# Performance work log

Measured on AMD Instinct MI355X. Metric: run time of the kernel, lower is better.

## Reference

```python
import jax, jax.numpy as jnp
import numpy as np
import math

B, S, D, H = 2, 2048, 1024, 16
DH = D // H  # head_size = 64


def setup_inputs() -> dict:
    key = jax.random.key(0)
    ks = jax.random.split(key, 11)
    s = 0.02
    return {
        "queries": jax.random.normal(ks[0], (B, S, D), jnp.float32),
        "keys": jax.random.normal(ks[1], (B, S, D), jnp.float32),
        "values": jax.random.normal(ks[2], (B, S, D), jnp.float32),
        # nn.Linear weights: y = x @ W.T + b, W has shape (out, in)
        "W_Q": jax.random.normal(ks[3], (D, D), jnp.float32) * s,
        "b_Q": jax.random.normal(ks[4], (D,), jnp.float32) * s,
        "W_K": jax.random.normal(ks[5], (D, D), jnp.float32) * s,
        "b_K": jax.random.normal(ks[6], (D,), jnp.float32) * s,
        "W_V": jax.random.normal(ks[7], (D, D), jnp.float32) * s,
        "b_V": jax.random.normal(ks[8], (D,), jnp.float32) * s,
        "W_O": jax.random.normal(ks[9], (D, D), jnp.float32) * s,
        "b_O": jax.random.normal(ks[10], (D,), jnp.float32) * s,
    }


def _split_heads(x):
    # (B, S, H*DH) -> (B, H, S, DH); torch.chunk+stack == reshape+transpose
    b, s, _ = x.shape
    return x.reshape(b, s, H, DH).transpose(0, 2, 1, 3)


def reference(queries, keys, values, W_Q, b_Q, W_K, b_K, W_V, b_V, W_O, b_O):
    q = _split_heads(queries @ W_Q.T + b_Q)  # (B,H,S,DH)
    k = _split_heads(keys @ W_K.T + b_K)
    v = _split_heads(values @ W_V.T + b_V)

    scale = 1.0 / math.sqrt(DH)
    scores = jnp.einsum("bhqd,bhkd->bhqk", q, k) * scale  # (B,H,S,S)
    causal = jnp.tril(jnp.ones((S, S), dtype=bool))  # allow j <= i (causal)
    scores = jnp.where(causal, scores, -jnp.inf)
    weights = jax.nn.softmax(scores, axis=-1)

    attended = jnp.einsum("bhqk,bhkd->bhqd", weights, v)  # (B,H,S,DH)
    merged = attended.transpose(0, 2, 1, 3).reshape(B, S, D)  # merge_heads
    return merged @ W_O.T + b_O
```

## Files before the change

kernel.cpp:

```cpp
#include <hip/hip_runtime.h>


typedef __bf16 bf16x8 __attribute__((ext_vector_type(8)));
typedef float  f32x4  __attribute__((ext_vector_type(4)));

#define B_  2
#define S_  2048
#define D_  1024
#define H_  16
#define DH_ 64

#define NEG_ 1.0e30f
#define M2_  5.77078016f
#define QSCALE_ 0.18033688f

#if __has_builtin(__builtin_amdgcn_exp2f)
#define EXP2(x) __builtin_amdgcn_exp2f(x)
#else
#define EXP2(x) __builtin_exp2f(x)
#endif

__device__ __forceinline__ void load_lds16(const __bf16* g, __bf16* lds_base) {
    __builtin_amdgcn_global_load_lds(
        (const __attribute__((address_space(1))) void*)g,
        (__attribute__((address_space(3))) void*)lds_base,
        16, 0, 0);
}

__device__ __forceinline__ bf16x8 cvt8(const float* __restrict__ p) {
    const float4 a = *(const float4*)p;
    const float4 b = *(const float4*)(p + 4);
    bf16x8 r;
    r[0] = (__bf16)a.x; r[1] = (__bf16)a.y; r[2] = (__bf16)a.z; r[3] = (__bf16)a.w;
    r[4] = (__bf16)b.x; r[5] = (__bf16)b.y; r[6] = (__bf16)b.z; r[7] = (__bf16)b.w;
    return r;
}

__global__ void cvt_kernel(const float* __restrict__ q, const float* __restrict__ k,
                           const float* __restrict__ v,
                           const float* __restrict__ wq, const float* __restrict__ wk,
                           const float* __restrict__ wv, const float* __restrict__ wo,
                           __bf16* __restrict__ qb, __bf16* __restrict__ kb,
                           __bf16* __restrict__ vb,
                           __bf16* __restrict__ wqb, __bf16* __restrict__ wkb,
                           __bf16* __restrict__ wvb, __bf16* __restrict__ wob) {
    const int z = blockIdx.z;
    const float* src; __bf16* dst; size_t n;
    switch (z) {
        case 0: src = q;  dst = qb;  n = (size_t)B_ * S_ * D_; break;
        case 1: src = k;  dst = kb;  n = (size_t)B_ * S_ * D_; break;
        case 2: src = v;  dst = vb;  n = (size_t)B_ * S_ * D_; break;
        case 3: src = wq; dst = wqb; n = (size_t)D_ * D_; break;
        case 4: src = wk; dst = wkb; n = (size_t)D_ * D_; break;
        case 5: src = wv; dst = wvb; n = (size_t)D_ * D_; break;
        default: src = wo; dst = wob; n = (size_t)D_ * D_; break;
    }
    const size_t i = ((size_t)blockIdx.x * 256 + threadIdx.x) * 8;
    if (i >= n) return;
    *(bf16x8*)(dst + i) = cvt8(src + i);
}

__device__ __forceinline__ void gemm128_bf(const __bf16* __restrict__ X,
                                           const __bf16* __restrict__ W,
                                           int m0, int n0, int K,
                                           __bf16* As, __bf16* Bs,
                                           f32x4 acc[4][4]) {
    const int tid  = threadIdx.x;
    const int wave = tid >> 6, lane = tid & 63;
    const int row  = lane & 15, quad = lane >> 4;
    const int wm   = wave >> 1, wn = wave & 1;
    const int arow = lane >> 2;
    const int acol = (lane & 3) * 8;

    const f32x4 fzero = {0.f, 0.f, 0.f, 0.f};
#pragma unroll
    for (int mt = 0; mt < 4; ++mt)
#pragma unroll
        for (int nt = 0; nt < 4; ++nt) acc[mt][nt] = fzero;

    auto stage = [&](int buf, int k0) {
#pragma unroll
        for (int c = 0; c < 2; ++c) {
            const int j = wave * 2 + c;
            load_lds16(X + (size_t)(m0 + j * 16 + arow) * K + k0 + acol,
                       As + buf * 4096 + j * 512);
            load_lds16(W + (size_t)(n0 + j * 16 + arow) * K + k0 + acol,
                       Bs + buf * 4096 + j * 512);
        }
    };

    stage(0, 0);
    int cur = 0;
    for (int k0 = 0; k0 < K; k0 += 32) {
        __syncthreads();
        if (k0 + 32 < K) stage(cur ^ 1, k0 + 32);
        const __bf16* Ab = As + cur * 4096;
        const __bf16* Bb = Bs + cur * 4096;
        bf16x8 af[4], bfv[4];
#pragma unroll
        for (int t = 0; t < 4; ++t) {
            af[t]  = *(const bf16x8*)(Ab + (wm * 64 + t * 16 + row) * 32 + quad * 8);
            bfv[t] = *(const bf16x8*)(Bb + (wn * 64 + t * 16 + row) * 32 + quad * 8);
        }
        __builtin_amdgcn_s_setprio(1);
#pragma unroll
        for (int mt = 0; mt < 4; ++mt)
#pragma unroll
            for (int nt = 0; nt < 4; ++nt)
                acc[mt][nt] = __builtin_amdgcn_mfma_f32_16x16x32_bf16(
                    af[mt], bfv[nt], acc[mt][nt], 0, 0, 0);
        __builtin_amdgcn_s_setprio(0);
        cur ^= 1;
    }
}

__global__ void qkv_kernel(const __bf16* __restrict__ qb, const __bf16* __restrict__ kb,
                           const __bf16* __restrict__ vb,
                           const __bf16* __restrict__ wqb, const __bf16* __restrict__ wkb,
                           const __bf16* __restrict__ wvb,
                           const float* __restrict__ bq, const float* __restrict__ bk,
                           const float* __restrict__ bv,
                           __bf16* __restrict__ q_ws, __bf16* __restrict__ k_ws,
                           __bf16* __restrict__ v_ws) {
    __shared__ __align__(16) __bf16 SMEM[16384];
    __bf16* As = SMEM;
    __bf16* Bs = SMEM + 8192;

    const int mode = blockIdx.z;
    const __bf16* X    = mode == 0 ? qb : mode == 1 ? kb : vb;
    const __bf16* W    = mode == 0 ? wqb : mode == 1 ? wkb : wvb;
    const float*  bias = mode == 0 ? bq : mode == 1 ? bk : bv;
    const int m0 = blockIdx.y * 128, n0 = blockIdx.x * 128;

    f32x4 acc[4][4];
    gemm128_bf(X, W, m0, n0, D_, As, Bs, acc);

    const int tid = threadIdx.x;
    const int wave = tid >> 6, lane = tid & 63;
    const int row = lane & 15, quad = lane >> 4;
    const int wm = wave >> 1, wn = wave & 1;

    if (mode == 2) {
        __syncthreads();
        __bf16* T = SMEM;
#pragma unroll
        for (int nt = 0; nt < 4; ++nt) {
            const int nloc = wn * 64 + nt * 16 + row;
            const float bf = bias[n0 + nloc];
#pragma unroll
            for (int mt = 0; mt < 4; ++mt)
#pragma unroll
                for (int r2 = 0; r2 < 4; ++r2) {
                    const int mloc = wm * 64 + mt * 16 + quad * 4 + r2;
                    T[nloc * 128 + ((((mloc >> 3) ^ (nloc & 15)) << 3) | (mloc & 7))] =
                        (__bf16)(acc[mt][nt][r2] + bf);
                }
        }
        __syncthreads();
#pragma unroll
        for (int p = 0; p < 8; ++p) {
            const int nloc = p * 16 + (tid >> 4);
            const int k = tid & 15;
            bf16x8 vv = *(const bf16x8*)(T + nloc * 128 + ((k ^ (nloc & 15)) << 3));
            const int n = n0 + nloc;
            const int h = n >> 6, dh = n & 63;
            const int m = m0 + k * 8;
            const int bb = m >> 11, s = m & (S_ - 1);
            *(bf16x8*)(v_ws + (((size_t)bb * H_ + h) * DH_ + dh) * S_ + s) = vv;
        }
        return;
    }

#pragma unroll
    for (int nt = 0; nt < 4; ++nt) {
        const int n  = n0 + wn * 64 + nt * 16 + row;
        const float bf = bias[n];
        const int h = n >> 6, dh = n & 63;
#pragma unroll
        for (int mt = 0; mt < 4; ++mt) {
#pragma unroll
            for (int r2 = 0; r2 < 4; ++r2) {
                const int m = m0 + wm * 64 + mt * 16 + quad * 4 + r2;
                const int bb = m >> 11, s = m & (S_ - 1);
                const float val = acc[mt][nt][r2] + bf;
                if (mode == 0)
                    q_ws[(((size_t)bb * H_ + h) * S_ + s) * DH_ + dh] = (__bf16)(val * QSCALE_);
                else
                    k_ws[(((size_t)bb * H_ + h) * S_ + s) * DH_ + dh] = (__bf16)val;
            }
        }
    }
}

__global__ __launch_bounds__(256, 4)
void attn_kernel(const __bf16* __restrict__ q_ws, const __bf16* __restrict__ k_ws,
                 const __bf16* __restrict__ v_ws, __bf16* __restrict__ att) {
    __shared__ __align__(16) __bf16 Ks[2 * 64 * 64];
    __shared__ __align__(16) __bf16 Vs[2 * 64 * 64];
    __shared__ __align__(16) __bf16 Ps[4 * 16 * 32];

    const int id = blockIdx.x;
    const int bh = (id & 7) * 4 + ((id >> 3) & 3);
    const int u = id >> 5, ua = u >> 3, uj = u & 7;
    const int qt = ua * 8 + ((ua & 1) ? (7 - uj) : uj);
    const int tid = threadIdx.x, wave = tid >> 6, lane = tid & 63;
    const int row = lane & 15, quad = lane >> 4;

    const __bf16* Qg = q_ws + ((size_t)bh * S_ + qt * 64 + wave * 16) * DH_;
    const __bf16* Kg = k_ws + (size_t)bh * S_ * DH_;
    const __bf16* Vg = v_ws + (size_t)bh * DH_ * S_;
    __bf16* Pw = Ps + wave * 512;

    bf16x8 qf[2];
#pragma unroll
    for (int ks = 0; ks < 2; ++ks)
        qf[ks] = *(const bf16x8*)(Qg + row * DH_ + ks * 32 + quad * 8);

    bf16x8 onesf;
#pragma unroll
    for (int i = 0; i < 8; ++i) onesf[i] = (__bf16)1.0f;

    const f32x4 fzero = {0.f, 0.f, 0.f, 0.f};
    f32x4 oacc[4];
    f32x4 lacc = fzero;
#pragma unroll
    for (int dt = 0; dt < 4; ++dt) oacc[dt] = fzero;

    const int srow = lane >> 3;
    const int scol = ((lane & 7) ^ srow) * 8;
    const int nkv = qt + 1;

    auto stage = [&](int buf, int kv) {
        __bf16* Kd = Ks + buf * 4096;
        __bf16* Vd = Vs + buf * 4096;
#pragma unroll
        for (int c = 0; c < 2; ++c) {
            const int ck = wave * 2 + c;
            load_lds16(Kg + (size_t)(kv * 64 + ck * 8 + srow) * DH_ + scol, Kd + ck * 512);
            load_lds16(Vg + (size_t)(ck * 8 + srow) * S_ + kv * 64 + scol, Vd + ck * 512);
        }
    };

    stage(0, 0);
    int cur = 0;
    for (int kv = 0; kv < nkv; ++kv) {
        __syncthreads();
        if (kv + 1 < nkv) stage(cur ^ 1, kv + 1);
        const bool diag = (kv == nkv - 1);
        const __bf16* Kb = Ks + cur * 4096;
        const __bf16* Vb = Vs + cur * 4096;
        const int swz = (row & 7) << 3;

#pragma unroll
        for (int kc = 0; kc < 2; ++kc) {
            f32x4 s[2];
            s[0] = fzero; s[1] = fzero;
            __builtin_amdgcn_s_setprio(1);
#pragma unroll
            for (int jn = 0; jn < 2; ++jn) {
                const int nt = kc * 2 + jn;
                const int kb = (nt * 16 + row) * 64 + quad * 8;
                bf16x8 kf0 = *(const bf16x8*)(Kb + (kb ^ swz));
                bf16x8 kf1 = *(const bf16x8*)(Kb + ((kb + 32) ^ swz));
                s[jn] = __builtin_amdgcn_mfma_f32_16x16x32_bf16(qf[0], kf0, s[jn], 0, 0, 0);
                s[jn] = __builtin_amdgcn_mfma_f32_16x16x32_bf16(qf[1], kf1, s[jn], 0, 0, 0);
            }
            __builtin_amdgcn_s_setprio(0);

            if (diag) {
#pragma unroll
                for (int jn = 0; jn < 2; ++jn) {
                    const int cloc = kc * 32 + jn * 16 + row;
#pragma unroll
                    for (int r = 0; r < 4; ++r) {
                        const int rloc = wave * 16 + quad * 4 + r;
                        if (cloc > rloc) s[jn][r] = -NEG_;
                    }
                }
            }

#pragma unroll
            for (int r = 0; r < 4; ++r)
#pragma unroll
                for (int jn = 0; jn < 2; ++jn) {
                    const float p = EXP2(s[jn][r] - M2_);
                    Pw[(((quad * 4 + r) * 32) + jn * 16 + row) ^ (quad << 3)] = (__bf16)p;
                }

            bf16x8 pf = *(const bf16x8*)(Pw + ((row * 32 + quad * 8) ^ (((row >> 2) & 3) << 3)));
            __builtin_amdgcn_s_setprio(1);
#pragma unroll
            for (int dt = 0; dt < 4; ++dt) {
                const int vb = (dt * 16 + row) * 64 + kc * 32 + quad * 8;
                bf16x8 vf = *(const bf16x8*)(Vb + (vb ^ swz));
                oacc[dt] = __builtin_amdgcn_mfma_f32_16x16x32_bf16(pf, vf, oacc[dt], 0, 0, 0);
            }
            lacc = __builtin_amdgcn_mfma_f32_16x16x32_bf16(pf, onesf, lacc, 0, 0, 0);
            __builtin_amdgcn_s_setprio(0);
        }
        cur ^= 1;
    }

    const int b = bh >> 4, h = bh & 15;
#pragma unroll
    for (int r = 0; r < 4; ++r) {
        const float inv = 1.f / lacc[r];
        const int s = qt * 64 + wave * 16 + quad * 4 + r;
#pragma unroll
        for (int dt = 0; dt < 4; ++dt) {
            att[((size_t)b * S_ + s) * D_ + h * DH_ + dt * 16 + row] =
                (__bf16)(oacc[dt][r] * inv);
        }
    }
}

__global__ void oproj_kernel(const __bf16* __restrict__ attn, const __bf16* __restrict__ wob,
                             const float* __restrict__ bo, float* __restrict__ out) {
    __shared__ __align__(16) __bf16 SMEM[16384];
    __bf16* As = SMEM;
    __bf16* Bs = SMEM + 8192;
    const int m0 = blockIdx.y * 128, n0 = blockIdx.x * 128;

    f32x4 acc[4][4];
    gemm128_bf(attn, wob, m0, n0, D_, As, Bs, acc);

    const int tid = threadIdx.x;
    const int wave = tid >> 6, lane = tid & 63;
    const int row = lane & 15, quad = lane >> 4;
    const int wm = wave >> 1, wn = wave & 1;

#pragma unroll
    for (int nt = 0; nt < 4; ++nt) {
        const int n = n0 + wn * 64 + nt * 16 + row;
        const float bf = bo[n];
#pragma unroll
        for (int mt = 0; mt < 4; ++mt) {
#pragma unroll
            for (int r = 0; r < 4; ++r) {
                const int m = m0 + wm * 64 + mt * 16 + quad * 4 + r;
                out[(size_t)m * D_ + n] = acc[mt][nt][r] + bf;
            }
        }
    }
}

extern "C" void kernel_launch(void* const* d_in, const int* in_sizes, int n_in,
                              void* d_out, int out_size, void* d_ws, size_t ws_size,
                              hipStream_t stream) {
    const float* q_in = (const float*)d_in[0];
    const float* k_in = (const float*)d_in[1];
    const float* v_in = (const float*)d_in[2];
    const float* wq   = (const float*)d_in[3];
    const float* bq   = (const float*)d_in[4];
    const float* wk   = (const float*)d_in[5];
    const float* bk   = (const float*)d_in[6];
    const float* wv   = (const float*)d_in[7];
    const float* bv   = (const float*)d_in[8];
    const float* wo   = (const float*)d_in[9];
    const float* bo   = (const float*)d_in[10];

    char* ws = (char*)d_ws;
    const size_t MB = 1024 * 1024;
    __bf16* qb   = (__bf16*)(ws);
    __bf16* kb   = (__bf16*)(ws + 8 * MB);
    __bf16* vb   = (__bf16*)(ws + 16 * MB);
    __bf16* wqb  = (__bf16*)(ws + 24 * MB);
    __bf16* wkb  = (__bf16*)(ws + 26 * MB);
    __bf16* wvb  = (__bf16*)(ws + 28 * MB);
    __bf16* wob  = (__bf16*)(ws + 30 * MB);
    __bf16* q_ws = (__bf16*)(ws + 32 * MB);
    __bf16* k_ws = (__bf16*)(ws + 40 * MB);
    __bf16* v_ws = (__bf16*)(ws + 48 * MB);
    __bf16* attb = qb;
    float*  out  = (float*)d_out;

    cvt_kernel<<<dim3(2048, 1, 7), 256, 0, stream>>>(
        q_in, k_in, v_in, wq, wk, wv, wo, qb, kb, vb, wqb, wkb, wvb, wob);
    qkv_kernel<<<dim3(D_ / 128, (B_ * S_) / 128, 3), 256, 0, stream>>>(
        qb, kb, vb, wqb, wkb, wvb, bq, bk, bv, q_ws, k_ws, v_ws);
    attn_kernel<<<dim3(32 * 32), 256, 0, stream>>>(q_ws, k_ws, v_ws, attb);
    oproj_kernel<<<dim3(D_ / 128, (B_ * S_) / 128), 256, 0, stream>>>(attb, wob, bo, out);
}
```

Before: 209.6 us.

## Transpose attention MFMAs and shuffle P in registers instead of LDS

Swaps the operand order of the QK^T and PV MFMAs so each lane holds a full query row's scores. The softmax probabilities can then be packed to bf16 and redistributed with permlane32/permlane16 swaps, with no round-trip through the per-wave LDS P buffer. This removes the LDS writes, the read and the Ps shared allocation. The output store becomes a vectorized 4-element bf16 write per lane, and the causal mask indexing is adjusted for the transposed layout. Correctness depends on the permlane swap pattern producing the right A-operand layout; a fallback to bpermute/swizzle is used if the builtins are missing.

```diff
diff --git a/kernel.cpp b/kernel.cpp
--- a/kernel.cpp
+++ b/kernel.cpp
@@ -2,7 +2,10 @@
 
 
 typedef __bf16 bf16x8 __attribute__((ext_vector_type(8)));
+typedef __bf16 bf16x4 __attribute__((ext_vector_type(4)));
 typedef float  f32x4  __attribute__((ext_vector_type(4)));
+typedef int    i32x2  __attribute__((ext_vector_type(2)));
+typedef int    i32x4  __attribute__((ext_vector_type(4)));
 
 #define B_  2
 #define S_  2048
@@ -25,6 +28,39 @@
         (const __attribute__((address_space(1))) void*)g,
         (__attribute__((address_space(3))) void*)lds_base,
         16, 0, 0);
+}
+
+__device__ __forceinline__ int pack_bf16(float lo, float hi) {
+    union { int u; __bf16 h[2]; } r;
+    r.h[0] = (__bf16)lo; r.h[1] = (__bf16)hi;
+    return r.u;
+}
+
+__device__ __forceinline__ void p32swap(int& a, int& b, int lane) {
+#if __has_builtin(__builtin_amdgcn_permlane32_swap)
+    i32x2 r = __builtin_amdgcn_permlane32_swap(a, b, false, false);
+    a = r[0]; b = r[1];
+#else
+    const int addr = ((lane ^ 32) & 63) << 2;
+    int ax = __builtin_amdgcn_ds_bpermute(addr, a);
+    int bx = __builtin_amdgcn_ds_bpermute(addr, b);
+    int na = (lane < 32) ? a : bx;
+    int nb = (lane < 32) ? ax : b;
+    a = na; b = nb;
+#endif
+}
+__device__ __forceinline__ void p16swap(int& a, int& b, int lane) {
+#if __has_builtin(__builtin_amdgcn_permlane16_swap)
+    i32x2 r = __builtin_amdgcn_permlane16_swap(a, b, false, false);
+    a = r[0]; b = r[1];
+#else
+    int as = __builtin_amdgcn_ds_swizzle(a, 0x401F);
+    int bs = __builtin_amdgcn_ds_swizzle(b, 0x401F);
+    const bool odd = (lane >> 4) & 1;
+    int na = odd ? bs : a;
+    int nb = odd ? b : as;
+    a = na; b = nb;
+#endif
 }
 
 __device__ __forceinline__ bf16x8 cvt8(const float* __restrict__ p) {
@@ -197,7 +233,6 @@
                  const __bf16* __restrict__ v_ws, __bf16* __restrict__ att) {
     __shared__ __align__(16) __bf16 Ks[2 * 64 * 64];
     __shared__ __align__(16) __bf16 Vs[2 * 64 * 64];
-    __shared__ __align__(16) __bf16 Ps[4 * 16 * 32];
 
     const int id = blockIdx.x;
     const int bh = (id & 7) * 4 + ((id >> 3) & 3);
@@ -209,7 +244,6 @@
     const __bf16* Qg = q_ws + ((size_t)bh * S_ + qt * 64 + wave * 16) * DH_;
     const __bf16* Kg = k_ws + (size_t)bh * S_ * DH_;
     const __bf16* Vg = v_ws + (size_t)bh * DH_ * S_;
-    __bf16* Pw = Ps + wave * 512;
 
     bf16x8 qf[2];
 #pragma unroll
@@ -262,55 +296,59 @@
                 const int kb = (nt * 16 + row) * 64 + quad * 8;
                 bf16x8 kf0 = *(const bf16x8*)(Kb + (kb ^ swz));
                 bf16x8 kf1 = *(const bf16x8*)(Kb + ((kb + 32) ^ swz));
-                s[jn] = __builtin_amdgcn_mfma_f32_16x16x32_bf16(qf[0], kf0, s[jn], 0, 0, 0);
-                s[jn] = __builtin_amdgcn_mfma_f32_16x16x32_bf16(qf[1], kf1, s[jn], 0, 0, 0);
+                s[jn] = __builtin_amdgcn_mfma_f32_16x16x32_bf16(kf0, qf[0], s[jn], 0, 0, 0);
+                s[jn] = __builtin_amdgcn_mfma_f32_16x16x32_bf16(kf1, qf[1], s[jn], 0, 0, 0);
             }
             __builtin_amdgcn_s_setprio(0);
 
             if (diag) {
-#pragma unroll
-                for (int jn = 0; jn < 2; ++jn) {
-                    const int cloc = kc * 32 + jn * 16 + row;
+                const int rloc = wave * 16 + row;
+#pragma unroll
+                for (int jn = 0; jn < 2; ++jn)
 #pragma unroll
                     for (int r = 0; r < 4; ++r) {
-                        const int rloc = wave * 16 + quad * 4 + r;
+                        const int cloc = kc * 32 + jn * 16 + quad * 4 + r;
                         if (cloc > rloc) s[jn][r] = -NEG_;
                     }
-                }
-            }
-
-#pragma unroll
-            for (int r = 0; r < 4; ++r)
-#pragma unroll
-                for (int jn = 0; jn < 2; ++jn) {
-                    const float p = EXP2(s[jn][r] - M2_);
-                    Pw[(((quad * 4 + r) * 32) + jn * 16 + row) ^ (quad << 3)] = (__bf16)p;
-                }
-
-            bf16x8 pf = *(const bf16x8*)(Pw + ((row * 32 + quad * 8) ^ (((row >> 2) & 3) << 3)));
+            }
+
+            float p0[4], p1[4];
+#pragma unroll
+            for (int r = 0; r < 4; ++r) {
+                p0[r] = EXP2(s[0][r] - M2_);
+                p1[r] = EXP2(s[1][r] - M2_);
+            }
+            int a0 = pack_bf16(p0[0], p0[1]), a1 = pack_bf16(p0[2], p0[3]);
+            int b0 = pack_bf16(p1[0], p1[1]), b1 = pack_bf16(p1[2], p1[3]);
+            p32swap(a0, b0, lane); p16swap(a0, b0, lane);
+            p32swap(a1, b1, lane); p16swap(a1, b1, lane);
+            union { i32x4 i; bf16x8 v; } pu;
+            pu.i = (i32x4){a0, a1, b0, b1};
+            const bf16x8 pf = pu.v;
+
             __builtin_amdgcn_s_setprio(1);
 #pragma unroll
             for (int dt = 0; dt < 4; ++dt) {
                 const int vb = (dt * 16 + row) * 64 + kc * 32 + quad * 8;
                 bf16x8 vf = *(const bf16x8*)(Vb + (vb ^ swz));
-                oacc[dt] = __builtin_amdgcn_mfma_f32_16x16x32_bf16(pf, vf, oacc[dt], 0, 0, 0);
-            }
-            lacc = __builtin_amdgcn_mfma_f32_16x16x32_bf16(pf, onesf, lacc, 0, 0, 0);
+                oacc[dt] = __builtin_amdgcn_mfma_f32_16x16x32_bf16(vf, pf, oacc[dt], 0, 0, 0);
+            }
+            lacc = __builtin_amdgcn_mfma_f32_16x16x32_bf16(onesf, pf, lacc, 0, 0, 0);
             __builtin_amdgcn_s_setprio(0);
         }
         cur ^= 1;
     }
 
     const int b = bh >> 4, h = bh & 15;
-#pragma unroll
-    for (int r = 0; r < 4; ++r) {
-        const float inv = 1.f / lacc[r];
-        const int s = qt * 64 + wave * 16 + quad * 4 + r;
-#pragma unroll
-        for (int dt = 0; dt < 4; ++dt) {
-            att[((size_t)b * S_ + s) * D_ + h * DH_ + dt * 16 + row] =
-                (__bf16)(oacc[dt][r] * inv);
-        }
+    const float inv = 1.f / lacc[0];
+    const int srow2 = qt * 64 + wave * 16 + row;
+    __bf16* obase = att + ((size_t)b * S_ + srow2) * D_ + h * DH_;
+#pragma unroll
+    for (int dt = 0; dt < 4; ++dt) {
+        bf16x4 o;
+#pragma unroll
+        for (int r = 0; r < 4; ++r) o[r] = (__bf16)(oacc[dt][r] * inv);
+        *(bf16x4*)(obase + dt * 16 + quad * 4) = o;
     }
 }
 
```

Result: no change. 209.2 us (-0.2%).
